# Optimization experiments

Measured on AMD Instinct MI355X. Metric: run time of the kernel, lower is better.

Reference implementation:

```python
import jax, jax.numpy as jnp
import numpy as np

N_NODES = 100000


def gcn_conv(x, src, dst, W, b, n_nodes):
    # PyG GCNConv: add self-loops, sym-normalize, transform then aggregate.
    loop = jnp.arange(n_nodes, dtype=src.dtype)
    s = jnp.concatenate([src, loop])
    d = jnp.concatenate([dst, loop])
    ones = jnp.ones(s.shape[0], dtype=x.dtype)
    deg = jax.ops.segment_sum(ones, d, num_segments=n_nodes)
    dinv = jnp.where(deg > 0, jax.lax.rsqrt(deg), 0.0)
    norm = dinv[s] * dinv[d]  # [E+N]
    h = x @ W                 # [N, out]
    msg = h[s] * norm[:, None]
    out = jax.ops.segment_sum(msg, d, num_segments=n_nodes)
    return out + b


def setup_inputs() -> dict:
    key = jax.random.key(0)
    ks = jax.random.split(key, 10)
    n, f = N_NODES, 128
    x = jax.random.normal(ks[0], (n, f), dtype=jnp.float32)
    edge_index = jax.random.randint(ks[1], (2, 1600000), 0, n, dtype=jnp.int64)

    def glorot(k, fin, fout):
        lim = float(np.sqrt(6.0 / (fin + fout)))
        return jax.random.uniform(k, (fin, fout), jnp.float32, -lim, lim)

    return {
        "x": x,
        "edge_index": edge_index,
        "W1": glorot(ks[2], f, 128), "b1": jnp.zeros((128,), jnp.float32),
        "W2": glorot(ks[3], 128, 64), "b2": jnp.zeros((64,), jnp.float32),
        "W3": glorot(ks[4], 64, 32), "b3": jnp.zeros((32,), jnp.float32),
        "Wc": glorot(ks[5], 64, 1), "bc": jnp.zeros((1,), jnp.float32),
    }


def reference(x, edge_index, W1, b1, W2, b2, W3, b3, Wc, bc):
    n = x.shape[0]
    src, dst = edge_index[0], edge_index[1]
    h = jax.nn.relu(gcn_conv(x, src, dst, W1, b1, n))   # dropout: eval mode
    h = jax.nn.relu(gcn_conv(h, src, dst, W2, b2, n))
    h = jax.nn.relu(gcn_conv(h, src, dst, W3, b3, n))
    edge_feat = jnp.concatenate([h[src], h[dst]], axis=1)  # [E, 64]
    return edge_feat @ Wc + bc
```

## Files before the change

kernel.cpp:

```cpp
#include <hip/hip_runtime.h>


typedef unsigned short u16;
typedef short bfrag __attribute__((ext_vector_type(8)));
typedef float ffrag __attribute__((ext_vector_type(4)));

#define BSHIFT 8
#define MAXB   512
#define BIN_CHUNK 4096
#define BCAP   4608

static __device__ __forceinline__ float4 f4add(float4 a, float4 b) {
    return make_float4(a.x + b.x, a.y + b.y, a.z + b.z, a.w + b.w);
}

static __device__ __forceinline__ u16 f2bf(float f) {
    unsigned u = __float_as_uint(f);
    u = (u + 0x7FFFu + ((u >> 16) & 1u)) >> 16;
    return (u16)u;
}

static __device__ __forceinline__ void bfacc2(float& a0, float& a1, unsigned u) {
    a0 += __uint_as_float(u << 16);
    a1 += __uint_as_float(u & 0xFFFF0000u);
}


__global__ __launch_bounds__(256) void init_cursors(int* __restrict__ bcur, int B) {
    int i = blockIdx.x * 256 + threadIdx.x;
    if (i < B) bcur[i] = i * BCAP;
}

__global__ __launch_bounds__(256) void bin_edges(const int* __restrict__ src,
                                                 const int* __restrict__ dst,
                                                 int* __restrict__ bcur,
                                                 unsigned* __restrict__ pairs,
                                                 int E, int B) {
    __shared__ int h[MAXB];
    __shared__ int base[MAXB];
    const int t = threadIdx.x;
    const int e0 = blockIdx.x * BIN_CHUNK;
    const int eEnd = min(e0 + BIN_CHUNK, E);
    for (int i = t; i < B; i += 256) h[i] = 0;
    __syncthreads();
    for (int e = e0 + t; e < eEnd; e += 256)
        atomicAdd(&h[dst[e] >> BSHIFT], 1);
    __syncthreads();
    for (int i = t; i < B; i += 256) {
        int c = h[i];
        base[i] = c ? atomicAdd(&bcur[i], c) : 0;
        h[i] = 0;
    }
    __syncthreads();
    for (int e = e0 + t; e < eEnd; e += 256) {
        int d = dst[e];
        int b = d >> BSHIFT;
        int pos = base[b] + atomicAdd(&h[b], 1);
        pairs[pos] = ((unsigned)(d & 255) << 24) | (unsigned)src[e];
    }
}

__global__ __launch_bounds__(256) void build_csr(const unsigned* __restrict__ pairs,
                                                 const int* __restrict__ bcur,
                                                 int* __restrict__ rowp,
                                                 int* __restrict__ rowe,
                                                 float* __restrict__ dinv,
                                                 int* __restrict__ ssrc, int N) {
    __shared__ int s[256];
    __shared__ int cur[256];
    const int t = threadIdx.x;
    const int b = blockIdx.x;
    const int eBeg = b * BCAP, eEnd = bcur[b];
    const int nodeBase = b << BSHIFT;
    s[t] = 0;
    __syncthreads();
    for (int e = eBeg + t; e < eEnd; e += 256)
        atomicAdd(&s[pairs[e] >> 24], 1);
    __syncthreads();
    const int v = s[t];
    #pragma unroll
    for (int off = 1; off < 256; off <<= 1) {
        int add = (t >= off) ? s[t - off] : 0;
        __syncthreads();
        s[t] += add;
        __syncthreads();
    }
    const int rp = eBeg + s[t] - v;
    const int node = nodeBase + t;
    if (node < N) {
        rowp[node] = rp;
        rowe[node] = rp + v;
        dinv[node] = rsqrtf((float)(v + 1));
    }
    cur[t] = rp;
    __syncthreads();
    for (int e = eBeg + t; e < eEnd; e += 256) {
        unsigned p = pairs[e];
        int pos = atomicAdd(&cur[p >> 24], 1);
        ssrc[pos] = (int)(p & 0xFFFFFFu);
    }
}

__global__ __launch_bounds__(256) void prep_w2(const float* __restrict__ W1,
                                               u16* __restrict__ W1t,
                                               const float* __restrict__ W2,
                                               u16* __restrict__ W2t) {
    int idx = blockIdx.x * 256 + threadIdx.x;
    if (idx < 128 * 128) {
        int n = idx >> 7, k = idx & 127;
        W1t[idx] = f2bf(W1[k * 128 + n]);
    } else if (idx < 128 * 128 + 64 * 128) {
        int j = idx - 128 * 128;
        int n = j >> 7, k = j & 127;
        W2t[j] = f2bf(W2[k * 64 + n]);
    }
}

template <int FIN, int FOUT, bool AF32, int MINW>
__global__ __launch_bounds__(256, MINW)
void gemm_mfma(const void* __restrict__ Xv, const u16* __restrict__ Wt,
               const float* __restrict__ dinv, u16* __restrict__ G, int N) {
    constexpr int NT = FOUT / 16;
    constexpr int KK = FIN / 32;
    constexpr int CB = FIN / 8;
    constexpr int ITER = (64 * CB) / 256;
    __shared__ __align__(16) u16 xs[64 * FIN];
    __shared__ float ldv[64];

    const int t = threadIdx.x;
    const int wave = t >> 6;
    const int lane = t & 63;
    const int l15 = lane & 15;
    const int quad = lane >> 4;
    const int r0 = blockIdx.x * 64;

    bfrag Bf[NT][KK];
    #pragma unroll
    for (int nt = 0; nt < NT; nt++)
        #pragma unroll
        for (int kk = 0; kk < KK; kk++)
            Bf[nt][kk] = *reinterpret_cast<const bfrag*>(
                &Wt[(size_t)(nt * 16 + l15) * FIN + kk * 32 + quad * 8]);

    if (t < 64) ldv[t] = (r0 + t < N) ? dinv[r0 + t] : 0.f;

    #pragma unroll
    for (int i = 0; i < ITER; i++) {
        int v = t + 256 * i;
        int row = v / CB;
        int cb = v - row * CB;
        uint4 pack = make_uint4(0, 0, 0, 0);
        if (r0 + row < N) {
            if (AF32) {
                const float* X = (const float*)Xv;
                const float4* p = reinterpret_cast<const float4*>(
                    &X[(size_t)(r0 + row) * FIN + cb * 8]);
                float4 lo = p[0], hi = p[1];
                pack.x = f2bf(lo.x) | ((unsigned)f2bf(lo.y) << 16);
                pack.y = f2bf(lo.z) | ((unsigned)f2bf(lo.w) << 16);
                pack.z = f2bf(hi.x) | ((unsigned)f2bf(hi.y) << 16);
                pack.w = f2bf(hi.z) | ((unsigned)f2bf(hi.w) << 16);
            } else {
                const u16* X = (const u16*)Xv;
                pack = *reinterpret_cast<const uint4*>(
                    &X[(size_t)(r0 + row) * FIN + cb * 8]);
            }
        }
        int cbs = cb ^ (row & 7);
        *reinterpret_cast<uint4*>(&xs[row * FIN + cbs * 8]) = pack;
    }
    __syncthreads();

    ffrag acc[NT];
    #pragma unroll
    for (int nt = 0; nt < NT; nt++) {
        acc[nt][0] = 0.f; acc[nt][1] = 0.f; acc[nt][2] = 0.f; acc[nt][3] = 0.f;
    }

    const int arow = wave * 16 + l15;
    #pragma unroll
    for (int kk = 0; kk < KK; kk++) {
        int cb = (kk * 4 + quad) ^ (l15 & 7);
        bfrag a = *reinterpret_cast<const bfrag*>(&xs[arow * FIN + cb * 8]);
        #pragma unroll
        for (int nt = 0; nt < NT; nt++)
            acc[nt] = __builtin_amdgcn_mfma_f32_16x16x32_bf16(a, Bf[nt][kk], acc[nt], 0, 0, 0);
    }

    #pragma unroll
    for (int nt = 0; nt < NT; nt++)
        #pragma unroll
        for (int r = 0; r < 4; r++) {
            int rl = wave * 16 + quad * 4 + r;
            int grow = r0 + rl;
            if (grow < N)
                G[(size_t)grow * FOUT + nt * 16 + l15] = f2bf(acc[nt][r] * ldv[rl]);
        }
}

template <int F, bool OUT_BF16>
__global__ __launch_bounds__(256) void aggregate_bf16(const u16* __restrict__ G,
                                                      const int* __restrict__ rowp,
                                                      const int* __restrict__ rowe,
                                                      const int* __restrict__ ssrc,
                                                      const float* __restrict__ dinv,
                                                      const float* __restrict__ bias,
                                                      void* __restrict__ Hout, int N) {
    constexpr int L = F / 8;
    constexpr int NPB = 256 / L;
    const int t = threadIdx.x;
    const int lj = t % L;
    const int d = blockIdx.x * NPB + t / L;
    if (d >= N) return;

    const uint4* G4 = reinterpret_cast<const uint4*>(G);
    float a[8];
    #pragma unroll
    for (int i = 0; i < 8; i++) a[i] = 0.f;
    {
        uint4 u = G4[(size_t)d * L + lj];
        bfacc2(a[0], a[1], u.x); bfacc2(a[2], a[3], u.y);
        bfacc2(a[4], a[5], u.z); bfacc2(a[6], a[7], u.w);
    }
    int e = rowp[d];
    const int end = rowe[d];
    for (; e + 4 <= end; e += 4) {
        int s0 = ssrc[e], s1 = ssrc[e + 1], s2 = ssrc[e + 2], s3 = ssrc[e + 3];
        uint4 u0 = G4[(size_t)s0 * L + lj];
        uint4 u1 = G4[(size_t)s1 * L + lj];
        uint4 u2 = G4[(size_t)s2 * L + lj];
        uint4 u3 = G4[(size_t)s3 * L + lj];
        bfacc2(a[0], a[1], u0.x); bfacc2(a[2], a[3], u0.y);
        bfacc2(a[4], a[5], u0.z); bfacc2(a[6], a[7], u0.w);
        bfacc2(a[0], a[1], u1.x); bfacc2(a[2], a[3], u1.y);
        bfacc2(a[4], a[5], u1.z); bfacc2(a[6], a[7], u1.w);
        bfacc2(a[0], a[1], u2.x); bfacc2(a[2], a[3], u2.y);
        bfacc2(a[4], a[5], u2.z); bfacc2(a[6], a[7], u2.w);
        bfacc2(a[0], a[1], u3.x); bfacc2(a[2], a[3], u3.y);
        bfacc2(a[4], a[5], u3.z); bfacc2(a[6], a[7], u3.w);
    }
    for (; e < end; e++) {
        uint4 u = G4[(size_t)ssrc[e] * L + lj];
        bfacc2(a[0], a[1], u.x); bfacc2(a[2], a[3], u.y);
        bfacc2(a[4], a[5], u.z); bfacc2(a[6], a[7], u.w);
    }
    const float dv = dinv[d];
    const float4 b0 = reinterpret_cast<const float4*>(bias)[lj * 2];
    const float4 b1 = reinterpret_cast<const float4*>(bias)[lj * 2 + 1];
    float h[8];
    h[0] = fmaxf(a[0] * dv + b0.x, 0.f);
    h[1] = fmaxf(a[1] * dv + b0.y, 0.f);
    h[2] = fmaxf(a[2] * dv + b0.z, 0.f);
    h[3] = fmaxf(a[3] * dv + b0.w, 0.f);
    h[4] = fmaxf(a[4] * dv + b1.x, 0.f);
    h[5] = fmaxf(a[5] * dv + b1.y, 0.f);
    h[6] = fmaxf(a[6] * dv + b1.z, 0.f);
    h[7] = fmaxf(a[7] * dv + b1.w, 0.f);
    if (OUT_BF16) {
        uint4 pk;
        pk.x = f2bf(h[0]) | ((unsigned)f2bf(h[1]) << 16);
        pk.y = f2bf(h[2]) | ((unsigned)f2bf(h[3]) << 16);
        pk.z = f2bf(h[4]) | ((unsigned)f2bf(h[5]) << 16);
        pk.w = f2bf(h[6]) | ((unsigned)f2bf(h[7]) << 16);
        reinterpret_cast<uint4*>(Hout)[(size_t)d * L + lj] = pk;
    } else {
        float4* H4 = reinterpret_cast<float4*>(Hout);
        H4[(size_t)d * (F / 4) + lj * 2]     = make_float4(h[0], h[1], h[2], h[3]);
        H4[(size_t)d * (F / 4) + lj * 2 + 1] = make_float4(h[4], h[5], h[6], h[7]);
    }
}

__global__ __launch_bounds__(256) void aggregate_l3s(const float* __restrict__ G,
                                                     const int* __restrict__ rowp,
                                                     const int* __restrict__ rowe,
                                                     const int* __restrict__ ssrc,
                                                     const float* __restrict__ dinv,
                                                     const float* __restrict__ bias,
                                                     const float* __restrict__ Wc,
                                                     float2* __restrict__ ab, int N) {
    constexpr int L = 8;
    const int t = threadIdx.x;
    const int lj = t % L;
    const int d = blockIdx.x * 32 + t / L;
    if (d >= N) return;

    const float4* G4 = reinterpret_cast<const float4*>(G);
    float4 acc = G4[(size_t)d * L + lj];
    int e = rowp[d];
    const int end = rowe[d];
    for (; e + 4 <= end; e += 4) {
        int s0 = ssrc[e], s1 = ssrc[e + 1], s2 = ssrc[e + 2], s3 = ssrc[e + 3];
        float4 v0 = G4[(size_t)s0 * L + lj];
        float4 v1 = G4[(size_t)s1 * L + lj];
        float4 v2 = G4[(size_t)s2 * L + lj];
        float4 v3 = G4[(size_t)s3 * L + lj];
        acc = f4add(acc, f4add(f4add(v0, v1), f4add(v2, v3)));
    }
    for (; e < end; e++)
        acc = f4add(acc, G4[(size_t)ssrc[e] * L + lj]);
    const float dv = dinv[d];
    const float4 b4 = reinterpret_cast<const float4*>(bias)[lj];
    float4 h;
    h.x = fmaxf(acc.x * dv + b4.x, 0.f);
    h.y = fmaxf(acc.y * dv + b4.y, 0.f);
    h.z = fmaxf(acc.z * dv + b4.z, 0.f);
    h.w = fmaxf(acc.w * dv + b4.w, 0.f);
    const float4 wa = reinterpret_cast<const float4*>(Wc)[lj];
    const float4 wb = reinterpret_cast<const float4*>(Wc + 32)[lj];
    float p = h.x * wa.x + h.y * wa.y + h.z * wa.z + h.w * wa.w;
    float q = h.x * wb.x + h.y * wb.y + h.z * wb.z + h.w * wb.w;
    p += __shfl_xor(p, 1); q += __shfl_xor(q, 1);
    p += __shfl_xor(p, 2); q += __shfl_xor(q, 2);
    p += __shfl_xor(p, 4); q += __shfl_xor(q, 4);
    if (lj == 0) ab[d] = make_float2(p, q);
}

template <int FIN, int FOUT, int JG, int JT, int ROWS>
__global__ __launch_bounds__(256) void gemm_dinv(const float* __restrict__ X,
                                                 const float* __restrict__ W,
                                                 const float* __restrict__ dinv,
                                                 float* __restrict__ G, int N) {
    constexpr int GROUPS = 256 / JG;
    constexpr int RPT = ROWS / GROUPS;
    __shared__ float xs[ROWS * FIN];
    const int t = threadIdx.x;
    const int r0 = blockIdx.x * ROWS;

    constexpr int NV = ROWS * FIN / 4;
    const float4* X4 = reinterpret_cast<const float4*>(X + (size_t)r0 * FIN);
    float4* xs4 = reinterpret_cast<float4*>(xs);
    #pragma unroll
    for (int v = t; v < NV; v += 256) {
        int row = v / (FIN / 4);
        float4 val = make_float4(0.f, 0.f, 0.f, 0.f);
        if (r0 + row < N) val = X4[v];
        xs4[v] = val;
    }
    __syncthreads();

    const int jg = t % JG;
    const int grp = t / JG;
    float acc[RPT][JT];
    #pragma unroll
    for (int r = 0; r < RPT; r++)
        #pragma unroll
        for (int jj = 0; jj < JT; jj++) acc[r][jj] = 0.f;

    #pragma unroll 2
    for (int k0 = 0; k0 < FIN; k0 += 8) {
        float wr[8][JT];
        #pragma unroll
        for (int q = 0; q < 8; q++)
            #pragma unroll
            for (int jj = 0; jj < JT; jj++)
                wr[q][jj] = W[(k0 + q) * FOUT + jg + jj * JG];
        #pragma unroll
        for (int r = 0; r < RPT; r++) {
            const int lr = grp * RPT + r;
            float xv[8];
            #pragma unroll
            for (int q = 0; q < 8; q++) xv[q] = xs[lr * FIN + k0 + q];
            #pragma unroll
            for (int q = 0; q < 8; q++)
                #pragma unroll
                for (int jj = 0; jj < JT; jj++)
                    acc[r][jj] += xv[q] * wr[q][jj];
        }
    }

    #pragma unroll
    for (int r = 0; r < RPT; r++) {
        const int gr = r0 + grp * RPT + r;
        if (gr < N) {
            const float dv = dinv[gr];
            #pragma unroll
            for (int jj = 0; jj < JT; jj++)
                G[(size_t)gr * FOUT + jg + jj * JG] = acc[r][jj] * dv;
        }
    }
}


__global__ __launch_bounds__(256) void edge_out(const int* __restrict__ src,
                                                const int* __restrict__ dst,
                                                const float2* __restrict__ ab,
                                                const float* __restrict__ bc,
                                                float* __restrict__ out, int E) {
    int e = blockIdx.x * 256 + threadIdx.x;
    if (e < E) out[e] = ab[src[e]].x + ab[dst[e]].y + bc[0];
}

extern "C" void kernel_launch(void* const* d_in, const int* in_sizes, int n_in,
                              void* d_out, int out_size, void* d_ws, size_t ws_size,
                              hipStream_t stream) {
    const float* x  = (const float*)d_in[0];
    const int*   ei = (const int*)d_in[1];
    const float* W1 = (const float*)d_in[2];
    const float* b1 = (const float*)d_in[3];
    const float* W2 = (const float*)d_in[4];
    const float* b2 = (const float*)d_in[5];
    const float* W3 = (const float*)d_in[6];
    const float* b3 = (const float*)d_in[7];
    const float* Wc = (const float*)d_in[8];
    const float* bc = (const float*)d_in[9];
    float* out = (float*)d_out;

    const int N = in_sizes[0] / 128;
    const int E = in_sizes[1] / 2;
    const int B = (N + 255) >> BSHIFT;
    const int* src = ei;
    const int* dst = ei + E;

    size_t off = 0;
    auto alloc = [&](size_t bytes) -> void* {
        size_t o = (off + 255) & ~(size_t)255;
        off = o + bytes;
        return (void*)((char*)d_ws + o);
    };
    float* dinv = (float*)alloc((size_t)N * 4);
    int*   rowp = (int*)alloc((size_t)N * 4);
    int*   rowe = (int*)alloc((size_t)N * 4);
    int*   bcur = (int*)alloc((size_t)(B + 1) * 4);
    int*   ssrc = (int*)alloc((size_t)B * BCAP * 4);
    u16*   w1t  = (u16*)alloc(128 * 128 * 2);
    u16*   w2t  = (u16*)alloc(128 * 64 * 2);
    u16*   g16  = (u16*)alloc((size_t)N * 128 * 2);
    u16*   h1b  = (u16*)alloc((size_t)N * 128 * 2);
    float* h2f  = (float*)alloc((size_t)N * 64 * 4);
    float2* ab  = (float2*)alloc((size_t)N * 8);
    (void)ws_size; (void)n_in; (void)out_size;

    unsigned* pairs = (unsigned*)h1b;
    float* g3f = (float*)g16;

    const int gE = (E + 255) / 256;
    const int gR = (N + 63) / 64;

    init_cursors<<<(B + 255) / 256, 256, 0, stream>>>(bcur, B);
    bin_edges<<<(E + BIN_CHUNK - 1) / BIN_CHUNK, 256, 0, stream>>>(src, dst, bcur, pairs, E, B);
    build_csr<<<B, 256, 0, stream>>>(pairs, bcur, rowp, rowe, dinv, ssrc, N);

    prep_w2<<<96, 256, 0, stream>>>(W1, w1t, W2, w2t);

    gemm_mfma<128, 128, true, 2><<<gR, 256, 0, stream>>>(x, w1t, dinv, g16, N);
    aggregate_bf16<128, true><<<(N + 15) / 16, 256, 0, stream>>>(g16, rowp, rowe, ssrc, dinv, b1, h1b, N);
    gemm_mfma<128, 64, false, 4><<<gR, 256, 0, stream>>>(h1b, w2t, dinv, g16, N);
    aggregate_bf16<64, false><<<(N + 31) / 32, 256, 0, stream>>>(g16, rowp, rowe, ssrc, dinv, b2, h2f, N);
    gemm_dinv<64, 32, 32, 1, 32><<<(N + 31) / 32, 256, 0, stream>>>(h2f, W3, dinv, g3f, N);
    aggregate_l3s<<<(N + 31) / 32, 256, 0, stream>>>(g3f, rowp, rowe, ssrc, dinv, b3, Wc, ab, N);

    edge_out<<<gE, 256, 0, stream>>>(src, dst, ab, bc, out, E);
}
```

Before: 349.0 us.

## Fuse layer aggregation with next layer's GEMM and merge prep kernels

The layer-1 aggregation now does the 128x64 layer-2 transform right away. Each node's aggregated row goes through shared memory and is multiplied by a bf16 W2 kept in LDS. The layer-2 aggregation likewise does the 64x32 layer-3 transform in fp32. This removes the h1 and h2 intermediate round trips through global memory and two GEMM launches, and the cursor init is folded into the weight prep kernel. The cost is that the small GEMMs run on scalar FMAs instead of MFMA, and each block has to load the weights into LDS.

```diff
diff --git a/kernel.cpp b/kernel.cpp
--- a/kernel.cpp
+++ b/kernel.cpp
@@ -20,16 +20,17 @@
     return (u16)u;
 }
 
+static __device__ __forceinline__ float bflo(unsigned u) {
+    return __uint_as_float(u << 16);
+}
+static __device__ __forceinline__ float bfhi(unsigned u) {
+    return __uint_as_float(u & 0xFFFF0000u);
+}
 static __device__ __forceinline__ void bfacc2(float& a0, float& a1, unsigned u) {
-    a0 += __uint_as_float(u << 16);
-    a1 += __uint_as_float(u & 0xFFFF0000u);
-}
-
-
-__global__ __launch_bounds__(256) void init_cursors(int* __restrict__ bcur, int B) {
-    int i = blockIdx.x * 256 + threadIdx.x;
-    if (i < B) bcur[i] = i * BCAP;
-}
+    a0 += bflo(u);
+    a1 += bfhi(u);
+}
+
 
 __global__ __launch_bounds__(256) void bin_edges(const int* __restrict__ src,
                                                  const int* __restrict__ dst,
@@ -101,19 +102,20 @@
     }
 }
 
-__global__ __launch_bounds__(256) void prep_w2(const float* __restrict__ W1,
-                                               u16* __restrict__ W1t,
-                                               const float* __restrict__ W2,
-                                               u16* __restrict__ W2t) {
+__global__ __launch_bounds__(256) void prep_all(const float* __restrict__ W1,
+                                                u16* __restrict__ w1t,
+                                                const float* __restrict__ W2,
+                                                u16* __restrict__ w2g,
+                                                int* __restrict__ bcur, int B) {
     int idx = blockIdx.x * 256 + threadIdx.x;
     if (idx < 128 * 128) {
         int n = idx >> 7, k = idx & 127;
-        W1t[idx] = f2bf(W1[k * 128 + n]);
-    } else if (idx < 128 * 128 + 64 * 128) {
+        w1t[idx] = f2bf(W1[k * 128 + n]);
+    } else if (idx < 128 * 128 + 128 * 64) {
         int j = idx - 128 * 128;
-        int n = j >> 7, k = j & 127;
-        W2t[j] = f2bf(W2[k * 64 + n]);
-    }
+        w2g[j] = f2bf(W2[j]);
+    }
+    if (idx < B) bcur[idx] = idx * BCAP;
 }
 
 template <int FIN, int FOUT, bool AF32, int MINW>
@@ -198,19 +200,27 @@
         }
 }
 
-template <int F, bool OUT_BF16>
-__global__ __launch_bounds__(256) void aggregate_bf16(const u16* __restrict__ G,
-                                                      const int* __restrict__ rowp,
-                                                      const int* __restrict__ rowe,
-                                                      const int* __restrict__ ssrc,
-                                                      const float* __restrict__ dinv,
-                                                      const float* __restrict__ bias,
-                                                      void* __restrict__ Hout, int N) {
-    constexpr int L = F / 8;
-    constexpr int NPB = 256 / L;
-    const int t = threadIdx.x;
-    const int lj = t % L;
-    const int d = blockIdx.x * NPB + t / L;
+__global__ __launch_bounds__(256) void agg1_gemm2(const u16* __restrict__ G,
+                                                  const int* __restrict__ rowp,
+                                                  const int* __restrict__ rowe,
+                                                  const int* __restrict__ ssrc,
+                                                  const float* __restrict__ dinv,
+                                                  const float* __restrict__ bias,
+                                                  const u16* __restrict__ w2g,
+                                                  u16* __restrict__ g2, int N) {
+    __shared__ __align__(16) u16 wl[128 * 64];
+    __shared__ __align__(16) u16 hl[16][128];
+    const int t = threadIdx.x;
+    {
+        const uint4* s4 = reinterpret_cast<const uint4*>(w2g);
+        uint4* d4 = reinterpret_cast<uint4*>(wl);
+        #pragma unroll
+        for (int i = 0; i < 4; i++) d4[t + 256 * i] = s4[t + 256 * i];
+    }
+    __syncthreads();
+    const int lj = t & 15;
+    const int dn = t >> 4;
+    const int d = blockIdx.x * 16 + dn;
     if (d >= N) return;
 
     const uint4* G4 = reinterpret_cast<const uint4*>(G);
@@ -218,7 +228,7 @@
     #pragma unroll
     for (int i = 0; i < 8; i++) a[i] = 0.f;
     {
-        uint4 u = G4[(size_t)d * L + lj];
+        uint4 u = G4[(size_t)d * 16 + lj];
         bfacc2(a[0], a[1], u.x); bfacc2(a[2], a[3], u.y);
         bfacc2(a[4], a[5], u.z); bfacc2(a[6], a[7], u.w);
     }
@@ -226,10 +236,10 @@
     const int end = rowe[d];
     for (; e + 4 <= end; e += 4) {
         int s0 = ssrc[e], s1 = ssrc[e + 1], s2 = ssrc[e + 2], s3 = ssrc[e + 3];
-        uint4 u0 = G4[(size_t)s0 * L + lj];
-        uint4 u1 = G4[(size_t)s1 * L + lj];
-        uint4 u2 = G4[(size_t)s2 * L + lj];
-        uint4 u3 = G4[(size_t)s3 * L + lj];
+        uint4 u0 = G4[(size_t)s0 * 16 + lj];
+        uint4 u1 = G4[(size_t)s1 * 16 + lj];
+        uint4 u2 = G4[(size_t)s2 * 16 + lj];
+        uint4 u3 = G4[(size_t)s3 * 16 + lj];
         bfacc2(a[0], a[1], u0.x); bfacc2(a[2], a[3], u0.y);
         bfacc2(a[4], a[5], u0.z); bfacc2(a[6], a[7], u0.w);
         bfacc2(a[0], a[1], u1.x); bfacc2(a[2], a[3], u1.y);
@@ -240,7 +250,7 @@
         bfacc2(a[4], a[5], u3.z); bfacc2(a[6], a[7], u3.w);
     }
     for (; e < end; e++) {
-        uint4 u = G4[(size_t)ssrc[e] * L + lj];
+        uint4 u = G4[(size_t)ssrc[e] * 16 + lj];
         bfacc2(a[0], a[1], u.x); bfacc2(a[2], a[3], u.y);
         bfacc2(a[4], a[5], u.z); bfacc2(a[6], a[7], u.w);
     }
@@ -256,18 +266,118 @@
     h[5] = fmaxf(a[5] * dv + b1.y, 0.f);
     h[6] = fmaxf(a[6] * dv + b1.z, 0.f);
     h[7] = fmaxf(a[7] * dv + b1.w, 0.f);
-    if (OUT_BF16) {
-        uint4 pk;
-        pk.x = f2bf(h[0]) | ((unsigned)f2bf(h[1]) << 16);
-        pk.y = f2bf(h[2]) | ((unsigned)f2bf(h[3]) << 16);
-        pk.z = f2bf(h[4]) | ((unsigned)f2bf(h[5]) << 16);
-        pk.w = f2bf(h[6]) | ((unsigned)f2bf(h[7]) << 16);
-        reinterpret_cast<uint4*>(Hout)[(size_t)d * L + lj] = pk;
-    } else {
-        float4* H4 = reinterpret_cast<float4*>(Hout);
-        H4[(size_t)d * (F / 4) + lj * 2]     = make_float4(h[0], h[1], h[2], h[3]);
-        H4[(size_t)d * (F / 4) + lj * 2 + 1] = make_float4(h[4], h[5], h[6], h[7]);
-    }
+    uint4 pk;
+    pk.x = f2bf(h[0]) | ((unsigned)f2bf(h[1]) << 16);
+    pk.y = f2bf(h[2]) | ((unsigned)f2bf(h[3]) << 16);
+    pk.z = f2bf(h[4]) | ((unsigned)f2bf(h[5]) << 16);
+    pk.w = f2bf(h[6]) | ((unsigned)f2bf(h[7]) << 16);
+    *reinterpret_cast<uint4*>(&hl[dn][lj * 8]) = pk;
+    float g0 = 0.f, g1 = 0.f, g2v = 0.f, g3 = 0.f;
+    #pragma unroll 4
+    for (int kk = 0; kk < 16; kk++) {
+        uint4 hv = *reinterpret_cast<const uint4*>(&hl[dn][kk * 8]);
+        unsigned hw[4] = {hv.x, hv.y, hv.z, hv.w};
+        #pragma unroll
+        for (int p = 0; p < 4; p++) {
+            float hA = bflo(hw[p]);
+            float hB = bfhi(hw[p]);
+            int k0 = kk * 8 + p * 2;
+            uint2 wA = *reinterpret_cast<const uint2*>(&wl[k0 * 64 + lj * 4]);
+            uint2 wB = *reinterpret_cast<const uint2*>(&wl[(k0 + 1) * 64 + lj * 4]);
+            g0 += hA * bflo(wA.x); g1 += hA * bfhi(wA.x);
+            g2v += hA * bflo(wA.y); g3 += hA * bfhi(wA.y);
+            g0 += hB * bflo(wB.x); g1 += hB * bfhi(wB.x);
+            g2v += hB * bflo(wB.y); g3 += hB * bfhi(wB.y);
+        }
+    }
+    uint2 o;
+    o.x = f2bf(g0 * dv) | ((unsigned)f2bf(g1 * dv) << 16);
+    o.y = f2bf(g2v * dv) | ((unsigned)f2bf(g3 * dv) << 16);
+    *reinterpret_cast<uint2*>(&g2[(size_t)d * 64 + lj * 4]) = o;
+}
+
+__global__ __launch_bounds__(256) void agg2_gemm3(const u16* __restrict__ G,
+                                                  const int* __restrict__ rowp,
+                                                  const int* __restrict__ rowe,
+                                                  const int* __restrict__ ssrc,
+                                                  const float* __restrict__ dinv,
+                                                  const float* __restrict__ bias,
+                                                  const float* __restrict__ W3,
+                                                  float* __restrict__ g3, int N) {
+    __shared__ __align__(16) float wl[64 * 32];
+    __shared__ __align__(16) float hl[32][64];
+    const int t = threadIdx.x;
+    {
+        const float4* s4 = reinterpret_cast<const float4*>(W3);
+        float4* d4 = reinterpret_cast<float4*>(wl);
+        d4[t] = s4[t];
+        d4[t + 256] = s4[t + 256];
+    }
+    __syncthreads();
+    const int lj = t & 7;
+    const int dn = t >> 3;
+    const int d = blockIdx.x * 32 + dn;
+    if (d >= N) return;
+
+    const uint4* G4 = reinterpret_cast<const uint4*>(G);
+    float a[8];
+    #pragma unroll
+    for (int i = 0; i < 8; i++) a[i] = 0.f;
+    {
+        uint4 u = G4[(size_t)d * 8 + lj];
+        bfacc2(a[0], a[1], u.x); bfacc2(a[2], a[3], u.y);
+        bfacc2(a[4], a[5], u.z); bfacc2(a[6], a[7], u.w);
+    }
+    int e = rowp[d];
+    const int end = rowe[d];
+    for (; e + 4 <= end; e += 4) {
+        int s0 = ssrc[e], s1 = ssrc[e + 1], s2 = ssrc[e + 2], s3 = ssrc[e + 3];
+        uint4 u0 = G4[(size_t)s0 * 8 + lj];
+        uint4 u1 = G4[(size_t)s1 * 8 + lj];
+        uint4 u2 = G4[(size_t)s2 * 8 + lj];
+        uint4 u3 = G4[(size_t)s3 * 8 + lj];
+        bfacc2(a[0], a[1], u0.x); bfacc2(a[2], a[3], u0.y);
+        bfacc2(a[4], a[5], u0.z); bfacc2(a[6], a[7], u0.w);
+        bfacc2(a[0], a[1], u1.x); bfacc2(a[2], a[3], u1.y);
+        bfacc2(a[4], a[5], u1.z); bfacc2(a[6], a[7], u1.w);
+        bfacc2(a[0], a[1], u2.x); bfacc2(a[2], a[3], u2.y);
+        bfacc2(a[4], a[5], u2.z); bfacc2(a[6], a[7], u2.w);
+        bfacc2(a[0], a[1], u3.x); bfacc2(a[2], a[3], u3.y);
+        bfacc2(a[4], a[5], u3.z); bfacc2(a[6], a[7], u3.w);
+    }
+    for (; e < end; e++) {
+        uint4 u = G4[(size_t)ssrc[e] * 8 + lj];
+        bfacc2(a[0], a[1], u.x); bfacc2(a[2], a[3], u.y);
+        bfacc2(a[4], a[5], u.z); bfacc2(a[6], a[7], u.w);
+    }
+    const float dv = dinv[d];
+    const float4 b0 = reinterpret_cast<const float4*>(bias)[lj * 2];
+    const float4 b1 = reinterpret_cast<const float4*>(bias)[lj * 2 + 1];
+    float h[8];
+    h[0] = fmaxf(a[0] * dv + b0.x, 0.f);
+    h[1] = fmaxf(a[1] * dv + b0.y, 0.f);
+    h[2] = fmaxf(a[2] * dv + b0.z, 0.f);
+    h[3] = fmaxf(a[3] * dv + b0.w, 0.f);
+    h[4] = fmaxf(a[4] * dv + b1.x, 0.f);
+    h[5] = fmaxf(a[5] * dv + b1.y, 0.f);
+    h[6] = fmaxf(a[6] * dv + b1.z, 0.f);
+    h[7] = fmaxf(a[7] * dv + b1.w, 0.f);
+    *reinterpret_cast<float4*>(&hl[dn][lj * 8])     = make_float4(h[0], h[1], h[2], h[3]);
+    *reinterpret_cast<float4*>(&hl[dn][lj * 8 + 4]) = make_float4(h[4], h[5], h[6], h[7]);
+    float g[4] = {0.f, 0.f, 0.f, 0.f};
+    #pragma unroll 4
+    for (int k4 = 0; k4 < 16; k4++) {
+        float4 hv = *reinterpret_cast<const float4*>(&hl[dn][k4 * 4]);
+        float hs[4] = {hv.x, hv.y, hv.z, hv.w};
+        #pragma unroll
+        for (int p = 0; p < 4; p++) {
+            float4 w = *reinterpret_cast<const float4*>(&wl[(k4 * 4 + p) * 32 + lj * 4]);
+            g[0] += hs[p] * w.x; g[1] += hs[p] * w.y;
+            g[2] += hs[p] * w.z; g[3] += hs[p] * w.w;
+        }
+    }
+    *reinterpret_cast<float4*>(&g3[(size_t)d * 32 + lj * 4]) =
+        make_float4(g[0] * dv, g[1] * dv, g[2] * dv, g[3] * dv);
 }
 
 __global__ __launch_bounds__(256) void aggregate_l3s(const float* __restrict__ G,
@@ -315,71 +425,6 @@
     if (lj == 0) ab[d] = make_float2(p, q);
 }
 
-template <int FIN, int FOUT, int JG, int JT, int ROWS>
-__global__ __launch_bounds__(256) void gemm_dinv(const float* __restrict__ X,
-                                                 const float* __restrict__ W,
-                                                 const float* __restrict__ dinv,
-                                                 float* __restrict__ G, int N) {
-    constexpr int GROUPS = 256 / JG;
-    constexpr int RPT = ROWS / GROUPS;
-    __shared__ float xs[ROWS * FIN];
-    const int t = threadIdx.x;
-    const int r0 = blockIdx.x * ROWS;
-
-    constexpr int NV = ROWS * FIN / 4;
-    const float4* X4 = reinterpret_cast<const float4*>(X + (size_t)r0 * FIN);
-    float4* xs4 = reinterpret_cast<float4*>(xs);
-    #pragma unroll
-    for (int v = t; v < NV; v += 256) {
-        int row = v / (FIN / 4);
-        float4 val = make_float4(0.f, 0.f, 0.f, 0.f);
-        if (r0 + row < N) val = X4[v];
-        xs4[v] = val;
-    }
-    __syncthreads();
-
-    const int jg = t % JG;
-    const int grp = t / JG;
-    float acc[RPT][JT];
-    #pragma unroll
-    for (int r = 0; r < RPT; r++)
-        #pragma unroll
-        for (int jj = 0; jj < JT; jj++) acc[r][jj] = 0.f;
-
-    #pragma unroll 2
-    for (int k0 = 0; k0 < FIN; k0 += 8) {
-        float wr[8][JT];
-        #pragma unroll
-        for (int q = 0; q < 8; q++)
-            #pragma unroll
-            for (int jj = 0; jj < JT; jj++)
-                wr[q][jj] = W[(k0 + q) * FOUT + jg + jj * JG];
-        #pragma unroll
-        for (int r = 0; r < RPT; r++) {
-            const int lr = grp * RPT + r;
-            float xv[8];
-            #pragma unroll
-            for (int q = 0; q < 8; q++) xv[q] = xs[lr * FIN + k0 + q];
-            #pragma unroll
-            for (int q = 0; q < 8; q++)
-                #pragma unroll
-                for (int jj = 0; jj < JT; jj++)
-                    acc[r][jj] += xv[q] * wr[q][jj];
-        }
-    }
-
-    #pragma unroll
-    for (int r = 0; r < RPT; r++) {
-        const int gr = r0 + grp * RPT + r;
-        if (gr < N) {
-            const float dv = dinv[gr];
-            #pragma unroll
-            for (int jj = 0; jj < JT; jj++)
-                G[(size_t)gr * FOUT + jg + jj * JG] = acc[r][jj] * dv;
-        }
-    }
-}
-
 
 __global__ __launch_bounds__(256) void edge_out(const int* __restrict__ src,
                                                 const int* __restrict__ dst,
@@ -423,30 +468,25 @@
     int*   bcur = (int*)alloc((size_t)(B + 1) * 4);
     int*   ssrc = (int*)alloc((size_t)B * BCAP * 4);
     u16*   w1t  = (u16*)alloc(128 * 128 * 2);
-    u16*   w2t  = (u16*)alloc(128 * 64 * 2);
+    u16*   w2g  = (u16*)alloc(128 * 64 * 2);
     u16*   g16  = (u16*)alloc((size_t)N * 128 * 2);
-    u16*   h1b  = (u16*)alloc((size_t)N * 128 * 2);
-    float* h2f  = (float*)alloc((size_t)N * 64 * 4);
+    u16*   g2b  = (u16*)alloc((size_t)N * 64 * 2);
     float2* ab  = (float2*)alloc((size_t)N * 8);
     (void)ws_size; (void)n_in; (void)out_size;
 
-    unsigned* pairs = (unsigned*)h1b;
+    unsigned* pairs = (unsigned*)g2b;
     float* g3f = (float*)g16;
 
     const int gE = (E + 255) / 256;
     const int gR = (N + 63) / 64;
 
-    init_cursors<<<(B + 255) / 256, 256, 0, stream>>>(bcur, B);
+    prep_all<<<96, 256, 0, stream>>>(W1, w1t, W2, w2g, bcur, B);
     bin_edges<<<(E + BIN_CHUNK - 1) / BIN_CHUNK, 256, 0, stream>>>(src, dst, bcur, pairs, E, B);
     build_csr<<<B, 256, 0, stream>>>(pairs, bcur, rowp, rowe, dinv, ssrc, N);
 
-    prep_w2<<<96, 256, 0, stream>>>(W1, w1t, W2, w2t);
-
     gemm_mfma<128, 128, true, 2><<<gR, 256, 0, stream>>>(x, w1t, dinv, g16, N);
-    aggregate_bf16<128, true><<<(N + 15) / 16, 256, 0, stream>>>(g16, rowp, rowe, ssrc, dinv, b1, h1b, N);
-    gemm_mfma<128, 64, false, 4><<<gR, 256, 0, stream>>>(h1b, w2t, dinv, g16, N);
-    aggregate_bf16<64, false><<<(N + 31) / 32, 256, 0, stream>>>(g16, rowp, rowe, ssrc, dinv, b2, h2f, N);
-    gemm_dinv<64, 32, 32, 1, 32><<<(N + 31) / 32, 256, 0, stream>>>(h2f, W3, dinv, g3f, N);
+    agg1_gemm2<<<(N + 15) / 16, 256, 0, stream>>>(g16, rowp, rowe, ssrc, dinv, b1, w2g, g2b, N);
+    agg2_gemm3<<<(N + 31) / 32, 256, 0, stream>>>(g2b, rowp, rowe, ssrc, dinv, b2, W3, g3f, N);
     aggregate_l3s<<<(N + 31) / 32, 256, 0, stream>>>(g3f, rowp, rowe, ssrc, dinv, b3, Wc, ab, N);
 
     edge_out<<<gE, 256, 0, stream>>>(src, dst, ab, bc, out, E);
```

New measurement: 340.4 us. -2.5%, faster.
